# Performance work log

Hardware: AMD Instinct MI355X
Metric: run time of the kernel (lower is better)

Reference implementation:

```python
import jax, jax.numpy as jnp
import numpy as np

H = 8          # num_heads
D_MODEL = 512  # hidden_dim
HEAD_DIM = D_MODEL // H
SCALE = HEAD_DIM ** -0.5
N = 4096
NUM_GRAPHS = 32
NEG_INF = jnp.float32(-jnp.inf)


def setup_inputs() -> dict:
    key = jax.random.key(0)
    ks = jax.random.split(key, 12)
    w_std = D_MODEL ** -0.5  # ~ torch Linear init scale
    inp = {
        "x": jax.random.normal(ks[0], (N, D_MODEL), jnp.float32),
        "attention_bias": jax.random.normal(ks[1], (H, N, N), jnp.float32),
        "batch": jnp.sort(jax.random.randint(ks[2], (N,), 0, NUM_GRAPHS)),
        "Wq": jax.random.normal(ks[3], (D_MODEL, D_MODEL), jnp.float32) * w_std,
        "bq": jax.random.normal(ks[4], (D_MODEL,), jnp.float32) * w_std,
        "Wk": jax.random.normal(ks[5], (D_MODEL, D_MODEL), jnp.float32) * w_std,
        "bk": jax.random.normal(ks[6], (D_MODEL,), jnp.float32) * w_std,
        "Wv": jax.random.normal(ks[7], (D_MODEL, D_MODEL), jnp.float32) * w_std,
        "bv": jax.random.normal(ks[8], (D_MODEL,), jnp.float32) * w_std,
        "Wo": jax.random.normal(ks[9], (D_MODEL, D_MODEL), jnp.float32) * w_std,
        "bo": jax.random.normal(ks[10], (D_MODEL,), jnp.float32) * w_std,
    }
    return inp


def reference(x, attention_bias, batch, Wq, bq, Wk, bk, Wv, bv, Wo, bo):
    n = x.shape[0]
    # projections (torch Linear: y = x @ W.T + b)
    q = (x @ Wq.T + bq).reshape(n, H, HEAD_DIM)
    k = (x @ Wk.T + bk).reshape(n, H, HEAD_DIM)
    v = (x @ Wv.T + bv).reshape(n, H, HEAD_DIM)
    # scores [H, N, N] with relative-PE bias
    attn = jnp.einsum("nhd,mhd->hnm", q, k) * SCALE + attention_bias
    # batch mask: attend only within the same graph
    batch_mask = batch[:, None] != batch[None, :]  # [N, N], True = masked
    attn = jnp.where(batch_mask[None, :, :], NEG_INF, attn)
    attn = jax.nn.softmax(attn, axis=-1)
    attn = jnp.nan_to_num(attn, nan=0.0)
    # dropout is identity in eval / dropout=0.0
    out = jnp.einsum("hnm,mhd->nhd", attn, v).reshape(n, D_MODEL)
    out = out @ Wo.T + bo
    return out
```

## Files before the change

### kernel.cpp

```cpp
#include <hip/hip_runtime.h>

#define NTOK 4096
#define DMODEL 512
#define NHEAD 8
#define HDIM 64
#define KDIM 512
#define KITER (KDIM / 64)

typedef __bf16 bf16x8 __attribute__((ext_vector_type(8)));
typedef float f32x4 __attribute__((ext_vector_type(4)));
typedef unsigned short u16x8 __attribute__((ext_vector_type(8)));
typedef unsigned short u16x4 __attribute__((ext_vector_type(4)));

#define NEGINF (-__builtin_inff())

__device__ __forceinline__ f32x4 mfma16(bf16x8 a, bf16x8 b, f32x4 c) {
  return __builtin_amdgcn_mfma_f32_16x16x32_bf16(a, b, c, 0, 0, 0);
}

__device__ __forceinline__ unsigned short f2bf(float f) {
  unsigned u = __builtin_bit_cast(unsigned, f);
  u += 0x7FFFu + ((u >> 16) & 1u);
  return (unsigned short)(u >> 16);
}

__device__ __forceinline__ void gload_lds16(const void* g, void* l) {
  __builtin_amdgcn_global_load_lds(
      (const __attribute__((address_space(1))) void*)g,
      (__attribute__((address_space(3))) void*)l, 16, 0, 0);
}

__global__ void convert_kernel(const float* __restrict__ x,
                               const float* __restrict__ Wq, const float* __restrict__ bq,
                               const float* __restrict__ Wk, const float* __restrict__ bk,
                               const float* __restrict__ Wv, const float* __restrict__ bv,
                               const float* __restrict__ Wo,
                               const int* __restrict__ batch,
                               unsigned short* __restrict__ xb,
                               unsigned short* __restrict__ wqkv,
                               unsigned short* __restrict__ wo,
                               float* __restrict__ bqkv,
                               int* __restrict__ qrange) {
  __shared__ int bsh[NTOK];
  if (blockIdx.x == 0) {
    for (int i = threadIdx.x; i < NTOK; i += 256) bsh[i] = batch[i];
  }
  const int XV = NTOK * DMODEL / 4;
  const int WV = DMODEL * DMODEL / 4;
  const int total = XV + 4 * WV + 1536 / 4;
  for (int i = blockIdx.x * blockDim.x + threadIdx.x; i < total;
       i += gridDim.x * blockDim.x) {
    if (i < XV) {
      float4 v = ((const float4*)x)[i];
      u16x4 pk = {f2bf(v.x), f2bf(v.y), f2bf(v.z), f2bf(v.w)};
      *(u16x4*)(xb + (size_t)i * 4) = pk;
    } else if (i < XV + 3 * WV) {
      int j = i - XV;
      const float* W; float sc; int jj;
      if (j < WV)          { W = Wq; sc = 0.125f; jj = j; }
      else if (j < 2 * WV) { W = Wk; sc = 1.0f;  jj = j - WV; }
      else                 { W = Wv; sc = 1.0f;  jj = j - 2 * WV; }
      float4 v = ((const float4*)W)[jj];
      u16x4 pk = {f2bf(v.x * sc), f2bf(v.y * sc), f2bf(v.z * sc), f2bf(v.w * sc)};
      *(u16x4*)(wqkv + (size_t)j * 4) = pk;
    } else if (i < XV + 4 * WV) {
      int j = i - XV - 3 * WV;
      float4 v = ((const float4*)Wo)[j];
      u16x4 pk = {f2bf(v.x), f2bf(v.y), f2bf(v.z), f2bf(v.w)};
      *(u16x4*)(wo + (size_t)j * 4) = pk;
    } else {
      int j = (i - XV - 4 * WV) * 4;
      #pragma unroll
      for (int t = 0; t < 4; ++t) {
        int e = j + t;
        float v = (e < 512) ? bq[e] * 0.125f
                 : (e < 1024 ? bk[e - 512] : bv[e - 1024]);
        bqkv[e] = v;
      }
    }
  }
  if (blockIdx.x == 0) {
    __syncthreads();
    if (threadIdx.x < 256) {
      int q0 = threadIdx.x * 16;
      int blo = bsh[q0];
      int bhi = bsh[q0 + 15];
      int lo = 0, hi = NTOK;
      while (lo < hi) { int m = (lo + hi) >> 1; if (bsh[m] < blo) lo = m + 1; else hi = m; }
      qrange[threadIdx.x * 2] = lo >> 6;
      lo = 0; hi = NTOK;
      while (lo < hi) { int m = (lo + hi) >> 1; if (bsh[m] < bhi + 1) lo = m + 1; else hi = m; }
      qrange[threadIdx.x * 2 + 1] = (lo + 63) >> 6;
    }
  }
}

#define BUFE (192 * 64)
#define BUFB (BUFE * 2)
template <int MODE>
__global__ __launch_bounds__(256) void gemm_kernel(
    const unsigned short* __restrict__ A,
    const unsigned short* __restrict__ B,
    const float* __restrict__ biasv,
    float* __restrict__ outf,
    unsigned short* __restrict__ qb,
    unsigned short* __restrict__ kb,
    unsigned short* __restrict__ vt) {
  __shared__ __align__(16) unsigned short lds[3 * BUFE];
  const int tid = threadIdx.x;
  const int lane = tid & 63;
  const int wv = tid >> 6;
  const int wm = wv >> 1, wn = wv & 1;
  const int r16 = lane & 15, g4 = lane >> 4;
  const int mt = blockIdx.x, nt = blockIdx.y;

  f32x4 acc[4][2];
  #pragma unroll
  for (int i = 0; i < 4; ++i)
    #pragma unroll
    for (int j = 0; j < 2; ++j)
      acc[i][j] = (f32x4){0.f, 0.f, 0.f, 0.f};

  const int srow = tid >> 3;
  const int scolb = (tid & 7) << 4;

#define STAGE(KT, BI)                                                        \
  {                                                                          \
    char* bA = (char*)lds + (BI) * BUFB;                                     \
    char* bB = bA + 128 * 128;                                               \
    _Pragma("unroll") for (int i = 0; i < 4; ++i) {                          \
      int row = i * 32 + srow;                                               \
      int cu_ = scolb ^ ((row & 7) << 4);                                    \
      gload_lds16(A + (size_t)(mt * 128 + row) * KDIM + (KT) * 64 + (cu_ >> 1), \
                  bA + i * 4096 + wv * 1024);                                \
    }                                                                        \
    _Pragma("unroll") for (int i = 0; i < 2; ++i) {                          \
      int row = i * 32 + srow;                                               \
      int cu_ = scolb ^ ((row & 7) << 4);                                    \
      gload_lds16(B + (size_t)(nt * 64 + row) * KDIM + (KT) * 64 + (cu_ >> 1), \
                  bB + i * 4096 + wv * 1024);                                \
    }                                                                        \
  }

#define COMPUTE(BI)                                                          \
  {                                                                          \
    const char* base = (const char*)lds + (BI) * BUFB;                       \
    _Pragma("unroll") for (int ks = 0; ks < 2; ++ks) {                       \
      bf16x8 af[4], bfr[2];                                                  \
      _Pragma("unroll") for (int f = 0; f < 4; ++f) {                        \
        int ra = wm * 64 + f * 16 + r16;                                     \
        af[f] = *(const bf16x8*)(base + ra * 128 +                           \
                                 ((ks * 64 + g4 * 16) ^ ((ra & 7) << 4)));   \
      }                                                                      \
      _Pragma("unroll") for (int f = 0; f < 2; ++f) {                        \
        int rb = wn * 32 + f * 16 + r16;                                     \
        bfr[f] = *(const bf16x8*)(base + 128 * 128 + rb * 128 +              \
                                  ((ks * 64 + g4 * 16) ^ ((rb & 7) << 4)));  \
      }                                                                      \
      _Pragma("unroll") for (int fm = 0; fm < 4; ++fm)                       \
        _Pragma("unroll") for (int fn = 0; fn < 2; ++fn)                     \
          acc[fm][fn] = mfma16(af[fm], bfr[fn], acc[fm][fn]);                \
    }                                                                        \
  }

  STAGE(0, 0);
  STAGE(1, 1);
  int cur = 0;
  #pragma unroll
  for (int kt = 0; kt < KITER; ++kt) {
    if (kt < KITER - 1) {
      asm volatile("s_waitcnt vmcnt(6)" ::: "memory");
    } else {
      asm volatile("s_waitcnt vmcnt(0)" ::: "memory");
    }
    __builtin_amdgcn_s_barrier();
    if (kt + 2 < KITER) {
      int bi = cur ? cur - 1 : 2;
      STAGE(kt + 2, bi);
    }
    COMPUTE(cur);
    cur = (cur == 2) ? 0 : cur + 1;
  }
#undef STAGE
#undef COMPUTE

  #pragma unroll
  for (int fm = 0; fm < 4; ++fm) {
    #pragma unroll
    for (int fn = 0; fn < 2; ++fn) {
      int mb = mt * 128 + wm * 64 + fm * 16 + g4 * 4;
      int n = nt * 64 + wn * 32 + fn * 16 + r16;
      float bv = biasv[n];
      if (MODE == 1) {
        #pragma unroll
        for (int r = 0; r < 4; ++r)
          outf[(size_t)(mb + r) * DMODEL + n] = acc[fm][fn][r] + bv;
      } else {
        if (n < 512) {
          #pragma unroll
          for (int r = 0; r < 4; ++r)
            qb[(size_t)(mb + r) * DMODEL + n] = f2bf(acc[fm][fn][r] + bv);
        } else if (n < 1024) {
          int nn = n - 512;
          #pragma unroll
          for (int r = 0; r < 4; ++r)
            kb[(size_t)(mb + r) * DMODEL + nn] = f2bf(acc[fm][fn][r] + bv);
        } else {
          int nn = n - 1024;
          u16x4 pk;
          #pragma unroll
          for (int r = 0; r < 4; ++r) pk[r] = f2bf(acc[fm][fn][r] + bv);
          *(u16x4*)(vt + (size_t)nn * NTOK + mb) = pk;
        }
      }
    }
  }
}

__global__ __launch_bounds__(64) void attn_kernel(
    const unsigned short* __restrict__ qb,
    const unsigned short* __restrict__ kb,
    const unsigned short* __restrict__ vt,
    const float* __restrict__ bias,
    const int* __restrict__ batch,
    const int* __restrict__ qrange,
    unsigned short* __restrict__ ao) {
  __shared__ __align__(16) unsigned short pl[16 * 72];
  const int lane = threadIdx.x & 63;
  const int r16 = lane & 15, g4 = lane >> 4;
  const int h = blockIdx.x & 7;
  const int qt = blockIdx.x >> 3;
  const int qrow0 = qt * 16;
  const int hoff = h * HDIM;

  const unsigned short* qrow = qb + (size_t)(qrow0 + r16) * DMODEL + hoff + g4 * 8;
  bf16x8 qa0 = *(const bf16x8*)qrow;
  bf16x8 qa1 = *(const bf16x8*)(qrow + 32);

  int qbt[4];
  const float* bprow[4];
  const float* bh = bias + (size_t)h * NTOK * NTOK;
  #pragma unroll
  for (int r = 0; r < 4; ++r) {
    qbt[r] = batch[qrow0 + g4 * 4 + r];
    bprow[r] = bh + (size_t)(qrow0 + g4 * 4 + r) * NTOK;
  }

  const int tile0 = qrange[qt * 2];
  const int tile1 = qrange[qt * 2 + 1];

  float m_r[4] = {NEGINF, NEGINF, NEGINF, NEGINF};
  float l_r[4] = {0.f, 0.f, 0.f, 0.f};
  f32x4 o[4];
  #pragma unroll
  for (int d = 0; d < 4; ++d) o[d] = (f32x4){0.f, 0.f, 0.f, 0.f};

#define PREFETCH_KB(T, K0, K1, BV, KBT)                                      \
  {                                                                          \
    int kvb_ = (T) << 6;                                                     \
    _Pragma("unroll") for (int c = 0; c < 4; ++c) {                          \
      const unsigned short* kp =                                             \
          kb + (size_t)(kvb_ + c * 16 + r16) * DMODEL + hoff + g4 * 8;       \
      K0[c] = *(const bf16x8*)kp;                                            \
      K1[c] = *(const bf16x8*)(kp + 32);                                     \
    }                                                                        \
    _Pragma("unroll") for (int c = 0; c < 4; ++c) {                          \
      KBT[c] = batch[kvb_ + c * 16 + r16];                                   \
      _Pragma("unroll") for (int r = 0; r < 4; ++r)                          \
        BV[c][r] = bprow[r][kvb_ + c * 16 + r16];                            \
    }                                                                        \
  }

#define TILE_STEP(T, K0C, K1C, BVC, KBTC, K0N, K1N, BVN, KBTN)               \
  {                                                                          \
    int kvb = (T) << 6;                                                      \
    f32x4 s[4];                                                              \
    _Pragma("unroll") for (int c = 0; c < 4; ++c) {                          \
      f32x4 z = (f32x4){0.f, 0.f, 0.f, 0.f};                                 \
      z = mfma16(qa0, K0C[c], z);                                            \
      z = mfma16(qa1, K1C[c], z);                                            \
      s[c] = z;                                                              \
    }                                                                        \
        \
    bf16x8 v0[4], v1[4];                                                     \
    _Pragma("unroll") for (int d = 0; d < 4; ++d) {                          \
      const unsigned short* vp =                                             \
          vt + (size_t)(hoff + d * 16 + r16) * NTOK + kvb + g4 * 8;          \
      v0[d] = *(const bf16x8*)vp;                                            \
      v1[d] = *(const bf16x8*)(vp + 32);                                     \
    }                                                                        \
     \
    {                                                                        \
      int tn_ = ((T) + 1 < tile1) ? (T) + 1 : (T);                           \
      PREFETCH_KB(tn_, K0N, K1N, BVN, KBTN);                                 \
    }                                                                        \
    _Pragma("unroll") for (int c = 0; c < 4; ++c)                            \
      _Pragma("unroll") for (int r = 0; r < 4; ++r)                          \
        s[c][r] = (qbt[r] == KBTC[c]) ? (s[c][r] + BVC[c][r]) : NEGINF;      \
    float scl[4];                                                            \
    _Pragma("unroll") for (int r = 0; r < 4; ++r) {                          \
      float tm = fmaxf(fmaxf(s[0][r], s[1][r]), fmaxf(s[2][r], s[3][r]));    \
      tm = fmaxf(tm, __shfl_xor(tm, 1));                                     \
      tm = fmaxf(tm, __shfl_xor(tm, 2));                                     \
      tm = fmaxf(tm, __shfl_xor(tm, 4));                                     \
      tm = fmaxf(tm, __shfl_xor(tm, 8));                                     \
      float mn = fmaxf(m_r[r], tm);                                          \
      bool dead = (mn == NEGINF);                                            \
      scl[r] = dead ? 1.0f : __expf(m_r[r] - mn);                            \
      m_r[r] = mn;                                                           \
      float rs = 0.f;                                                        \
      _Pragma("unroll") for (int c = 0; c < 4; ++c) {                        \
        float p = dead ? 0.0f : __expf(s[c][r] - mn);                        \
        s[c][r] = p;                                                         \
        rs += p;                                                             \
      }                                                                      \
      rs += __shfl_xor(rs, 1);                                               \
      rs += __shfl_xor(rs, 2);                                               \
      rs += __shfl_xor(rs, 4);                                               \
      rs += __shfl_xor(rs, 8);                                               \
      l_r[r] = l_r[r] * scl[r] + rs;                                         \
    }                                                                        \
    _Pragma("unroll") for (int c = 0; c < 4; ++c)                            \
      _Pragma("unroll") for (int r = 0; r < 4; ++r)                          \
        pl[(g4 * 4 + r) * 72 + c * 16 + r16] = f2bf(s[c][r]);                \
    asm volatile("" ::: "memory");                                           \
    u16x8 pr0 = *(const u16x8*)(pl + r16 * 72 + g4 * 8);                     \
    u16x8 pr1 = *(const u16x8*)(pl + r16 * 72 + 32 + g4 * 8);                \
    bf16x8 pa0 = __builtin_bit_cast(bf16x8, pr0);                            \
    bf16x8 pa1 = __builtin_bit_cast(bf16x8, pr1);                            \
    _Pragma("unroll") for (int d = 0; d < 4; ++d) {                          \
      _Pragma("unroll") for (int r = 0; r < 4; ++r) o[d][r] *= scl[r];       \
    }                                                                        \
    _Pragma("unroll") for (int d = 0; d < 4; ++d) {                          \
      o[d] = mfma16(pa0, v0[d], o[d]);                                       \
      o[d] = mfma16(pa1, v1[d], o[d]);                                       \
    }                                                                        \
  }

  bf16x8 ka0[4], ka1[4], kc0[4], kc1[4];
  float bva[4][4], bvb[4][4];
  int kta[4], ktb[4];
  PREFETCH_KB(tile0, ka0, ka1, bva, kta);
  int t = tile0;
  while (true) {
    TILE_STEP(t, ka0, ka1, bva, kta, kc0, kc1, bvb, ktb);
    if (++t >= tile1) break;
    TILE_STEP(t, kc0, kc1, bvb, ktb, ka0, ka1, bva, kta);
    if (++t >= tile1) break;
  }

  #pragma unroll
  for (int r = 0; r < 4; ++r) {
    float inv = (l_r[r] > 0.f) ? 1.0f / l_r[r] : 0.0f;
    #pragma unroll
    for (int d = 0; d < 4; ++d)
      ao[(size_t)(qrow0 + g4 * 4 + r) * DMODEL + hoff + d * 16 + r16] =
          f2bf(o[d][r] * inv);
  }
#undef PREFETCH_KB
#undef TILE_STEP
}

extern "C" void kernel_launch(void* const* d_in, const int* in_sizes, int n_in,
                              void* d_out, int out_size, void* d_ws, size_t ws_size,
                              hipStream_t stream) {
  const float* x  = (const float*)d_in[0];
  const float* ab = (const float*)d_in[1];
  const int* batch = (const int*)d_in[2];
  const float* Wq = (const float*)d_in[3];
  const float* bq = (const float*)d_in[4];
  const float* Wk = (const float*)d_in[5];
  const float* bk = (const float*)d_in[6];
  const float* Wv = (const float*)d_in[7];
  const float* bv = (const float*)d_in[8];
  const float* Wo = (const float*)d_in[9];
  const float* bo = (const float*)d_in[10];
  float* out = (float*)d_out;

  char* ws = (char*)d_ws;
  const size_t MB = 1024 * 1024;
  unsigned short* xb   = (unsigned short*)(ws);
  unsigned short* qb   = (unsigned short*)(ws + 4 * MB);
  unsigned short* kb   = (unsigned short*)(ws + 8 * MB);
  unsigned short* vt   = (unsigned short*)(ws + 12 * MB);
  unsigned short* aout = (unsigned short*)(ws + 16 * MB);
  unsigned short* wqkv = (unsigned short*)(ws + 20 * MB);
  unsigned short* wo   = (unsigned short*)(ws + 22 * MB);
  float* bqkv          = (float*)(ws + 23 * MB);
  int* qrange          = (int*)(ws + 23 * MB + 65536);

  convert_kernel<<<dim3(1024), dim3(256), 0, stream>>>(
      x, Wq, bq, Wk, bk, Wv, bv, Wo, batch, xb, wqkv, wo, bqkv, qrange);

  gemm_kernel<0><<<dim3(32, 24), dim3(256), 0, stream>>>(
      xb, wqkv, bqkv, nullptr, qb, kb, vt);

  attn_kernel<<<dim3(2048), dim3(64), 0, stream>>>(
      qb, kb, vt, ab, batch, qrange, aout);

  gemm_kernel<1><<<dim3(32, 8), dim3(256), 0, stream>>>(
      aout, wo, bo, out, nullptr, nullptr, nullptr);
}
```

Before: 54.11 us.

## Use double-buffered GEMM pipeline, smaller out-proj tiles, and MFMA priority hints

The GEMM drops from a three-buffer to a two-buffer LDS pipeline. The output projection uses 64-row tiles and twice as many blocks to fill more CUs. Launch bounds now request more resident blocks per CU. The attention kernel raises wave priority around its MFMA sections with s_setprio. Less prefetch depth may expose load latency in exchange for lower LDS use and higher occupancy.

```diff
diff --git a/kernel.cpp b/kernel.cpp
--- a/kernel.cpp
+++ b/kernel.cpp
@@ -95,10 +95,8 @@
   }
 }
 
-#define BUFE (192 * 64)
-#define BUFB (BUFE * 2)
 template <int MODE>
-__global__ __launch_bounds__(256) void gemm_kernel(
+__global__ __launch_bounds__(256, MODE ? 2 : 3) void gemm_kernel(
     const unsigned short* __restrict__ A,
     const unsigned short* __restrict__ B,
     const float* __restrict__ biasv,
@@ -106,7 +104,11 @@
     unsigned short* __restrict__ qb,
     unsigned short* __restrict__ kb,
     unsigned short* __restrict__ vt) {
-  __shared__ __align__(16) unsigned short lds[3 * BUFE];
+  constexpr int BM = MODE ? 64 : 128;
+  constexpr int FM = MODE ? 2 : 4;
+  constexpr int ALOADS = BM / 32;
+  constexpr int BUFBYTES = (BM + 64) * 64 * 2;
+  __shared__ __align__(16) unsigned short lds[(BM + 64) * 64 * 2];
   const int tid = threadIdx.x;
   const int lane = tid & 63;
   const int wv = tid >> 6;
@@ -114,9 +116,9 @@
   const int r16 = lane & 15, g4 = lane >> 4;
   const int mt = blockIdx.x, nt = blockIdx.y;
 
-  f32x4 acc[4][2];
-  #pragma unroll
-  for (int i = 0; i < 4; ++i)
+  f32x4 acc[FM][2];
+  #pragma unroll
+  for (int i = 0; i < FM; ++i)
     #pragma unroll
     for (int j = 0; j < 2; ++j)
       acc[i][j] = (f32x4){0.f, 0.f, 0.f, 0.f};
@@ -126,12 +128,12 @@
 
 #define STAGE(KT, BI)                                                        \
   {                                                                          \
-    char* bA = (char*)lds + (BI) * BUFB;                                     \
-    char* bB = bA + 128 * 128;                                               \
-    _Pragma("unroll") for (int i = 0; i < 4; ++i) {                          \
+    char* bA = (char*)lds + (BI) * BUFBYTES;                                 \
+    char* bB = bA + BM * 128;                                                \
+    _Pragma("unroll") for (int i = 0; i < ALOADS; ++i) {                     \
       int row = i * 32 + srow;                                               \
       int cu_ = scolb ^ ((row & 7) << 4);                                    \
-      gload_lds16(A + (size_t)(mt * 128 + row) * KDIM + (KT) * 64 + (cu_ >> 1), \
+      gload_lds16(A + (size_t)(mt * BM + row) * KDIM + (KT) * 64 + (cu_ >> 1), \
                   bA + i * 4096 + wv * 1024);                                \
     }                                                                        \
     _Pragma("unroll") for (int i = 0; i < 2; ++i) {                          \
@@ -144,51 +146,49 @@
 
 #define COMPUTE(BI)                                                          \
   {                                                                          \
-    const char* base = (const char*)lds + (BI) * BUFB;                       \
+    const char* base = (const char*)lds + (BI) * BUFBYTES;                   \
     _Pragma("unroll") for (int ks = 0; ks < 2; ++ks) {                       \
-      bf16x8 af[4], bfr[2];                                                  \
-      _Pragma("unroll") for (int f = 0; f < 4; ++f) {                        \
-        int ra = wm * 64 + f * 16 + r16;                                     \
+      bf16x8 af[FM], bfr[2];                                                 \
+      _Pragma("unroll") for (int f = 0; f < FM; ++f) {                       \
+        int ra = wm * (FM * 16) + f * 16 + r16;                              \
         af[f] = *(const bf16x8*)(base + ra * 128 +                           \
                                  ((ks * 64 + g4 * 16) ^ ((ra & 7) << 4)));   \
       }                                                                      \
       _Pragma("unroll") for (int f = 0; f < 2; ++f) {                        \
         int rb = wn * 32 + f * 16 + r16;                                     \
-        bfr[f] = *(const bf16x8*)(base + 128 * 128 + rb * 128 +              \
+        bfr[f] = *(const bf16x8*)(base + BM * 128 + rb * 128 +               \
                                   ((ks * 64 + g4 * 16) ^ ((rb & 7) << 4)));  \
       }                                                                      \
-      _Pragma("unroll") for (int fm = 0; fm < 4; ++fm)                       \
+      _Pragma("unroll") for (int fm = 0; fm < FM; ++fm)                      \
         _Pragma("unroll") for (int fn = 0; fn < 2; ++fn)                     \
           acc[fm][fn] = mfma16(af[fm], bfr[fn], acc[fm][fn]);                \
     }                                                                        \
   }
 
   STAGE(0, 0);
-  STAGE(1, 1);
-  int cur = 0;
   #pragma unroll
   for (int kt = 0; kt < KITER; ++kt) {
-    if (kt < KITER - 1) {
-      asm volatile("s_waitcnt vmcnt(6)" ::: "memory");
+    if (kt + 1 < KITER) {
+      __builtin_amdgcn_s_barrier();
+      STAGE(kt + 1, (kt + 1) & 1);
+      if constexpr (MODE == 0)
+        asm volatile("s_waitcnt vmcnt(6)" ::: "memory");
+      else
+        asm volatile("s_waitcnt vmcnt(4)" ::: "memory");
     } else {
       asm volatile("s_waitcnt vmcnt(0)" ::: "memory");
     }
     __builtin_amdgcn_s_barrier();
-    if (kt + 2 < KITER) {
-      int bi = cur ? cur - 1 : 2;
-      STAGE(kt + 2, bi);
-    }
-    COMPUTE(cur);
-    cur = (cur == 2) ? 0 : cur + 1;
+    COMPUTE(kt & 1);
   }
 #undef STAGE
 #undef COMPUTE
 
   #pragma unroll
-  for (int fm = 0; fm < 4; ++fm) {
+  for (int fm = 0; fm < FM; ++fm) {
     #pragma unroll
     for (int fn = 0; fn < 2; ++fn) {
-      int mb = mt * 128 + wm * 64 + fm * 16 + g4 * 4;
+      int mb = mt * BM + wm * (FM * 16) + fm * 16 + g4 * 4;
       int n = nt * 64 + wn * 32 + fn * 16 + r16;
       float bv = biasv[n];
       if (MODE == 1) {
@@ -275,12 +275,14 @@
   {                                                                          \
     int kvb = (T) << 6;                                                      \
     f32x4 s[4];                                                              \
+    __builtin_amdgcn_s_setprio(1);                                           \
     _Pragma("unroll") for (int c = 0; c < 4; ++c) {                          \
       f32x4 z = (f32x4){0.f, 0.f, 0.f, 0.f};                                 \
       z = mfma16(qa0, K0C[c], z);                                            \
       z = mfma16(qa1, K1C[c], z);                                            \
       s[c] = z;                                                              \
     }                                                                        \
+    __builtin_amdgcn_s_setprio(0);                                           \
         \
     bf16x8 v0[4], v1[4];                                                     \
     _Pragma("unroll") for (int d = 0; d < 4; ++d) {                          \
@@ -331,10 +333,12 @@
     _Pragma("unroll") for (int d = 0; d < 4; ++d) {                          \
       _Pragma("unroll") for (int r = 0; r < 4; ++r) o[d][r] *= scl[r];       \
     }                                                                        \
+    __builtin_amdgcn_s_setprio(1);                                           \
     _Pragma("unroll") for (int d = 0; d < 4; ++d) {                          \
       o[d] = mfma16(pa0, v0[d], o[d]);                                       \
       o[d] = mfma16(pa1, v1[d], o[d]);                                       \
     }                                                                        \
+    __builtin_amdgcn_s_setprio(0);                                           \
   }
 
   bf16x8 ka0[4], ka1[4], kc0[4], kc1[4];
@@ -398,6 +402,6 @@
   attn_kernel<<<dim3(2048), dim3(64), 0, stream>>>(
       qb, kb, vt, ab, batch, qrange, aout);
 
-  gemm_kernel<1><<<dim3(32, 8), dim3(256), 0, stream>>>(
+  gemm_kernel<1><<<dim3(64, 8), dim3(256), 0, stream>>>(
       aout, wo, bo, out, nullptr, nullptr, nullptr);
 }
```

Measured after the change: 51.65 us. 4.6% less time.

## Fuse fp32-to-bf16 conversion into GEMM loads and drop convert kernel

Applied to the files above, without the earlier changes.

Removes the separate convert kernel by having the QKV and output-projection GEMMs load fp32 inputs and weights directly into registers, convert them to bf16 and write them to LDS in a register-staged double buffer. The qrange binary search moves into one block of the QKV GEMM. The output GEMM switches to 64x64 tiles for more blocks, and the attention kernel raises wave priority around its MFMA sections. This saves a launch and an intermediate bf16 round trip, but each GEMM block now re-reads and re-converts fp32 data, doubling global load bytes and adding VALU conversion work in the main loop.

```diff
diff --git a/kernel.cpp b/kernel.cpp
--- a/kernel.cpp
+++ b/kernel.cpp
@@ -24,89 +24,28 @@
   return (unsigned short)(u >> 16);
 }
 
-__device__ __forceinline__ void gload_lds16(const void* g, void* l) {
-  __builtin_amdgcn_global_load_lds(
-      (const __attribute__((address_space(1))) void*)g,
-      (__attribute__((address_space(3))) void*)l, 16, 0, 0);
-}
-
-__global__ void convert_kernel(const float* __restrict__ x,
-                               const float* __restrict__ Wq, const float* __restrict__ bq,
-                               const float* __restrict__ Wk, const float* __restrict__ bk,
-                               const float* __restrict__ Wv, const float* __restrict__ bv,
-                               const float* __restrict__ Wo,
-                               const int* __restrict__ batch,
-                               unsigned short* __restrict__ xb,
-                               unsigned short* __restrict__ wqkv,
-                               unsigned short* __restrict__ wo,
-                               float* __restrict__ bqkv,
-                               int* __restrict__ qrange) {
-  __shared__ int bsh[NTOK];
-  if (blockIdx.x == 0) {
-    for (int i = threadIdx.x; i < NTOK; i += 256) bsh[i] = batch[i];
-  }
-  const int XV = NTOK * DMODEL / 4;
-  const int WV = DMODEL * DMODEL / 4;
-  const int total = XV + 4 * WV + 1536 / 4;
-  for (int i = blockIdx.x * blockDim.x + threadIdx.x; i < total;
-       i += gridDim.x * blockDim.x) {
-    if (i < XV) {
-      float4 v = ((const float4*)x)[i];
-      u16x4 pk = {f2bf(v.x), f2bf(v.y), f2bf(v.z), f2bf(v.w)};
-      *(u16x4*)(xb + (size_t)i * 4) = pk;
-    } else if (i < XV + 3 * WV) {
-      int j = i - XV;
-      const float* W; float sc; int jj;
-      if (j < WV)          { W = Wq; sc = 0.125f; jj = j; }
-      else if (j < 2 * WV) { W = Wk; sc = 1.0f;  jj = j - WV; }
-      else                 { W = Wv; sc = 1.0f;  jj = j - 2 * WV; }
-      float4 v = ((const float4*)W)[jj];
-      u16x4 pk = {f2bf(v.x * sc), f2bf(v.y * sc), f2bf(v.z * sc), f2bf(v.w * sc)};
-      *(u16x4*)(wqkv + (size_t)j * 4) = pk;
-    } else if (i < XV + 4 * WV) {
-      int j = i - XV - 3 * WV;
-      float4 v = ((const float4*)Wo)[j];
-      u16x4 pk = {f2bf(v.x), f2bf(v.y), f2bf(v.z), f2bf(v.w)};
-      *(u16x4*)(wo + (size_t)j * 4) = pk;
-    } else {
-      int j = (i - XV - 4 * WV) * 4;
-      #pragma unroll
-      for (int t = 0; t < 4; ++t) {
-        int e = j + t;
-        float v = (e < 512) ? bq[e] * 0.125f
-                 : (e < 1024 ? bk[e - 512] : bv[e - 1024]);
-        bqkv[e] = v;
-      }
-    }
-  }
-  if (blockIdx.x == 0) {
-    __syncthreads();
-    if (threadIdx.x < 256) {
-      int q0 = threadIdx.x * 16;
-      int blo = bsh[q0];
-      int bhi = bsh[q0 + 15];
-      int lo = 0, hi = NTOK;
-      while (lo < hi) { int m = (lo + hi) >> 1; if (bsh[m] < blo) lo = m + 1; else hi = m; }
-      qrange[threadIdx.x * 2] = lo >> 6;
-      lo = 0; hi = NTOK;
-      while (lo < hi) { int m = (lo + hi) >> 1; if (bsh[m] < bhi + 1) lo = m + 1; else hi = m; }
-      qrange[threadIdx.x * 2 + 1] = (lo + 63) >> 6;
-    }
-  }
-}
-
-#define BUFE (192 * 64)
-#define BUFB (BUFE * 2)
-template <int MODE>
-__global__ __launch_bounds__(256) void gemm_kernel(
-    const unsigned short* __restrict__ A,
-    const unsigned short* __restrict__ B,
-    const float* __restrict__ biasv,
-    float* __restrict__ outf,
+__device__ __forceinline__ int lbound(const int* __restrict__ b, int val) {
+  int lo = 0, hi = NTOK;
+  while (lo < hi) {
+    int mid = (lo + hi) >> 1;
+    if (b[mid] < val) lo = mid + 1; else hi = mid;
+  }
+  return lo;
+}
+
+#define BUFB0 (192 * 64 * 2)
+
+__global__ __launch_bounds__(256, 2) void gemm_qkv(
+    const float* __restrict__ x,
+    const float* __restrict__ Wq, const float* __restrict__ bq,
+    const float* __restrict__ Wk, const float* __restrict__ bk,
+    const float* __restrict__ Wv, const float* __restrict__ bvv,
+    const int* __restrict__ batch,
     unsigned short* __restrict__ qb,
     unsigned short* __restrict__ kb,
-    unsigned short* __restrict__ vt) {
-  __shared__ __align__(16) unsigned short lds[3 * BUFE];
+    unsigned short* __restrict__ vt,
+    int* __restrict__ qrange) {
+  __shared__ __align__(16) unsigned short lds[2 * 192 * 64];
   const int tid = threadIdx.x;
   const int lane = tid & 63;
   const int wv = tid >> 6;
@@ -114,6 +53,10 @@
   const int r16 = lane & 15, g4 = lane >> 4;
   const int mt = blockIdx.x, nt = blockIdx.y;
 
+  const float* WB = (nt < 8) ? Wq : (nt < 16 ? Wk : Wv);
+  const float wscale = (nt < 8) ? 0.125f : 1.0f;
+  const int wrow0 = (nt & 7) * 64;
+
   f32x4 acc[4][2];
   #pragma unroll
   for (int i = 0; i < 4; ++i)
@@ -122,29 +65,51 @@
       acc[i][j] = (f32x4){0.f, 0.f, 0.f, 0.f};
 
   const int srow = tid >> 3;
-  const int scolb = (tid & 7) << 4;
-
-#define STAGE(KT, BI)                                                        \
-  {                                                                          \
-    char* bA = (char*)lds + (BI) * BUFB;                                     \
+  const int c0 = (tid & 7) * 8;
+
+#define LOADR0(KT, RA, RB)                                                   \
+  {                                                                          \
+    _Pragma("unroll") for (int i = 0; i < 4; ++i) {                          \
+      int row = i * 32 + srow;                                               \
+      int cs = c0 ^ ((row & 7) * 8);                                         \
+      const float* src = x + (size_t)(mt * 128 + row) * KDIM + (KT) * 64 + cs;\
+      RA[2 * i]     = *(const f32x4*)src;                                    \
+      RA[2 * i + 1] = *(const f32x4*)(src + 4);                              \
+    }                                                                        \
+    _Pragma("unroll") for (int i = 0; i < 2; ++i) {                          \
+      int row = i * 32 + srow;                                               \
+      int cs = c0 ^ ((row & 7) * 8);                                         \
+      const float* src = WB + (size_t)(wrow0 + row) * KDIM + (KT) * 64 + cs; \
+      RB[2 * i]     = *(const f32x4*)src;                                    \
+      RB[2 * i + 1] = *(const f32x4*)(src + 4);                              \
+    }                                                                        \
+  }
+
+#define WRITER0(BI, RA, RB)                                                  \
+  {                                                                          \
+    char* bA = (char*)lds + (BI) * BUFB0;                                    \
     char* bB = bA + 128 * 128;                                               \
     _Pragma("unroll") for (int i = 0; i < 4; ++i) {                          \
-      int row = i * 32 + srow;                                               \
-      int cu_ = scolb ^ ((row & 7) << 4);                                    \
-      gload_lds16(A + (size_t)(mt * 128 + row) * KDIM + (KT) * 64 + (cu_ >> 1), \
-                  bA + i * 4096 + wv * 1024);                                \
+      u16x8 pk;                                                              \
+      _Pragma("unroll") for (int e = 0; e < 4; ++e) {                        \
+        pk[e]     = f2bf(RA[2 * i][e]);                                      \
+        pk[e + 4] = f2bf(RA[2 * i + 1][e]);                                  \
+      }                                                                      \
+      *(u16x8*)(bA + i * 4096 + tid * 16) = pk;                              \
     }                                                                        \
     _Pragma("unroll") for (int i = 0; i < 2; ++i) {                          \
-      int row = i * 32 + srow;                                               \
-      int cu_ = scolb ^ ((row & 7) << 4);                                    \
-      gload_lds16(B + (size_t)(nt * 64 + row) * KDIM + (KT) * 64 + (cu_ >> 1), \
-                  bB + i * 4096 + wv * 1024);                                \
-    }                                                                        \
-  }
-
-#define COMPUTE(BI)                                                          \
-  {                                                                          \
-    const char* base = (const char*)lds + (BI) * BUFB;                       \
+      u16x8 pk;                                                              \
+      _Pragma("unroll") for (int e = 0; e < 4; ++e) {                        \
+        pk[e]     = f2bf(RB[2 * i][e] * wscale);                             \
+        pk[e + 4] = f2bf(RB[2 * i + 1][e] * wscale);                         \
+      }                                                                      \
+      *(u16x8*)(bB + i * 4096 + tid * 16) = pk;                              \
+    }                                                                        \
+  }
+
+#define COMPUTE0(BI)                                                         \
+  {                                                                          \
+    const char* base = (const char*)lds + (BI) * BUFB0;                      \
     _Pragma("unroll") for (int ks = 0; ks < 2; ++ks) {                       \
       bf16x8 af[4], bfr[2];                                                  \
       _Pragma("unroll") for (int f = 0; f < 4; ++f) {                        \
@@ -163,26 +128,30 @@
     }                                                                        \
   }
 
-  STAGE(0, 0);
-  STAGE(1, 1);
-  int cur = 0;
-  #pragma unroll
-  for (int kt = 0; kt < KITER; ++kt) {
-    if (kt < KITER - 1) {
-      asm volatile("s_waitcnt vmcnt(6)" ::: "memory");
-    } else {
-      asm volatile("s_waitcnt vmcnt(0)" ::: "memory");
-    }
-    __builtin_amdgcn_s_barrier();
-    if (kt + 2 < KITER) {
-      int bi = cur ? cur - 1 : 2;
-      STAGE(kt + 2, bi);
-    }
-    COMPUTE(cur);
-    cur = (cur == 2) ? 0 : cur + 1;
-  }
-#undef STAGE
-#undef COMPUTE
+#define STEP0(KT, RA, RB, RAN, RBN, LAST)                                    \
+  __builtin_amdgcn_s_barrier();                 \
+  WRITER0((KT) & 1, RA, RB);                 \
+  if (!(LAST)) { LOADR0((KT) + 1, RAN, RBN); }                               \
+  __builtin_amdgcn_sched_barrier(0);                                         \
+  asm volatile("s_waitcnt lgkmcnt(0)" ::: "memory");                         \
+  __builtin_amdgcn_s_barrier();              \
+  __builtin_amdgcn_sched_barrier(0);                                         \
+  COMPUTE0((KT) & 1);
+
+  f32x4 rA0[8], rB0[4], rA1[8], rB1[4];
+  LOADR0(0, rA0, rB0);
+  STEP0(0, rA0, rB0, rA1, rB1, 0)
+  STEP0(1, rA1, rB1, rA0, rB0, 0)
+  STEP0(2, rA0, rB0, rA1, rB1, 0)
+  STEP0(3, rA1, rB1, rA0, rB0, 0)
+  STEP0(4, rA0, rB0, rA1, rB1, 0)
+  STEP0(5, rA1, rB1, rA0, rB0, 0)
+  STEP0(6, rA0, rB0, rA1, rB1, 0)
+  STEP0(7, rA1, rB1, rA0, rB0, 1)
+#undef LOADR0
+#undef WRITER0
+#undef COMPUTE0
+#undef STEP0
 
   #pragma unroll
   for (int fm = 0; fm < 4; ++fm) {
@@ -190,29 +159,153 @@
     for (int fn = 0; fn < 2; ++fn) {
       int mb = mt * 128 + wm * 64 + fm * 16 + g4 * 4;
       int n = nt * 64 + wn * 32 + fn * 16 + r16;
-      float bv = biasv[n];
-      if (MODE == 1) {
+      if (n < 512) {
+        float bval = bq[n] * 0.125f;
         #pragma unroll
         for (int r = 0; r < 4; ++r)
-          outf[(size_t)(mb + r) * DMODEL + n] = acc[fm][fn][r] + bv;
+          qb[(size_t)(mb + r) * DMODEL + n] = f2bf(acc[fm][fn][r] + bval);
+      } else if (n < 1024) {
+        int nn = n - 512;
+        float bval = bk[nn];
+        #pragma unroll
+        for (int r = 0; r < 4; ++r)
+          kb[(size_t)(mb + r) * DMODEL + nn] = f2bf(acc[fm][fn][r] + bval);
       } else {
-        if (n < 512) {
-          #pragma unroll
-          for (int r = 0; r < 4; ++r)
-            qb[(size_t)(mb + r) * DMODEL + n] = f2bf(acc[fm][fn][r] + bv);
-        } else if (n < 1024) {
-          int nn = n - 512;
-          #pragma unroll
-          for (int r = 0; r < 4; ++r)
-            kb[(size_t)(mb + r) * DMODEL + nn] = f2bf(acc[fm][fn][r] + bv);
-        } else {
-          int nn = n - 1024;
-          u16x4 pk;
-          #pragma unroll
-          for (int r = 0; r < 4; ++r) pk[r] = f2bf(acc[fm][fn][r] + bv);
-          *(u16x4*)(vt + (size_t)nn * NTOK + mb) = pk;
-        }
+        int nn = n - 1024;
+        float bval = bvv[nn];
+        u16x4 pk;
+        #pragma unroll
+        for (int r = 0; r < 4; ++r) pk[r] = f2bf(acc[fm][fn][r] + bval);
+        *(u16x4*)(vt + (size_t)nn * NTOK + mb) = pk;
       }
+    }
+  }
+
+  if (mt == 0 && nt == 0) {
+    int q0 = tid * 16;
+    if (tid < 256) {
+      int blo = batch[q0];
+      int bhi = batch[q0 + 15];
+      qrange[tid * 2]     = lbound(batch, blo) >> 6;
+      qrange[tid * 2 + 1] = (lbound(batch, bhi + 1) + 63) >> 6;
+    }
+  }
+}
+
+#define BUFB1 (128 * 64 * 2)
+
+__global__ __launch_bounds__(256, 2) void gemm_out(
+    const unsigned short* __restrict__ aout,
+    const float* __restrict__ Wo, const float* __restrict__ bo,
+    float* __restrict__ out) {
+  __shared__ __align__(16) unsigned short lds[2 * 128 * 64];
+  const int tid = threadIdx.x;
+  const int lane = tid & 63;
+  const int wv = tid >> 6;
+  const int wm = wv >> 1, wn = wv & 1;
+  const int r16 = lane & 15, g4 = lane >> 4;
+  const int mt = blockIdx.x, nt = blockIdx.y;
+
+  f32x4 acc[2][2];
+  #pragma unroll
+  for (int i = 0; i < 2; ++i)
+    #pragma unroll
+    for (int j = 0; j < 2; ++j)
+      acc[i][j] = (f32x4){0.f, 0.f, 0.f, 0.f};
+
+  const int srow = tid >> 3;
+  const int c0 = (tid & 7) * 8;
+
+#define LOADR1(KT, RA, RB)                                                   \
+  {                                                                          \
+    _Pragma("unroll") for (int i = 0; i < 2; ++i) {                          \
+      int row = i * 32 + srow;                                               \
+      int cs = c0 ^ ((row & 7) * 8);                                         \
+      RA[i] = *(const u16x8*)(aout + (size_t)(mt * 64 + row) * KDIM +        \
+                              (KT) * 64 + cs);                               \
+    }                                                                        \
+    _Pragma("unroll") for (int i = 0; i < 2; ++i) {                          \
+      int row = i * 32 + srow;                                               \
+      int cs = c0 ^ ((row & 7) * 8);                                         \
+      const float* src = Wo + (size_t)(nt * 64 + row) * KDIM + (KT) * 64 + cs;\
+      RB[2 * i]     = *(const f32x4*)src;                                    \
+      RB[2 * i + 1] = *(const f32x4*)(src + 4);                              \
+    }                                                                        \
+  }
+
+#define WRITER1(BI, RA, RB)                                                  \
+  {                                                                          \
+    char* bA = (char*)lds + (BI) * BUFB1;                                    \
+    char* bB = bA + 64 * 128;                                                \
+    _Pragma("unroll") for (int i = 0; i < 2; ++i)                            \
+      *(u16x8*)(bA + i * 4096 + tid * 16) = RA[i];                           \
+    _Pragma("unroll") for (int i = 0; i < 2; ++i) {                          \
+      u16x8 pk;                                                              \
+      _Pragma("unroll") for (int e = 0; e < 4; ++e) {                        \
+        pk[e]     = f2bf(RB[2 * i][e]);                                      \
+        pk[e + 4] = f2bf(RB[2 * i + 1][e]);                                  \
+      }                                                                      \
+      *(u16x8*)(bB + i * 4096 + tid * 16) = pk;                              \
+    }                                                                        \
+  }
+
+#define COMPUTE1(BI)                                                         \
+  {                                                                          \
+    const char* base = (const char*)lds + (BI) * BUFB1;                      \
+    _Pragma("unroll") for (int ks = 0; ks < 2; ++ks) {                       \
+      bf16x8 af[2], bfr[2];                                                  \
+      _Pragma("unroll") for (int f = 0; f < 2; ++f) {                        \
+        int ra = wm * 32 + f * 16 + r16;                                     \
+        af[f] = *(const bf16x8*)(base + ra * 128 +                           \
+                                 ((ks * 64 + g4 * 16) ^ ((ra & 7) << 4)));   \
+      }                                                                      \
+      _Pragma("unroll") for (int f = 0; f < 2; ++f) {                        \
+        int rb = wn * 32 + f * 16 + r16;                                     \
+        bfr[f] = *(const bf16x8*)(base + 64 * 128 + rb * 128 +               \
+                                  ((ks * 64 + g4 * 16) ^ ((rb & 7) << 4)));  \
+      }                                                                      \
+      _Pragma("unroll") for (int fm = 0; fm < 2; ++fm)                       \
+        _Pragma("unroll") for (int fn = 0; fn < 2; ++fn)                     \
+          acc[fm][fn] = mfma16(af[fm], bfr[fn], acc[fm][fn]);                \
+    }                                                                        \
+  }
+
+#define STEP1(KT, RA, RB, RAN, RBN, LAST)                                    \
+  __builtin_amdgcn_s_barrier();                                              \
+  WRITER1((KT) & 1, RA, RB);                                                 \
+  if (!(LAST)) { LOADR1((KT) + 1, RAN, RBN); }                               \
+  __builtin_amdgcn_sched_barrier(0);                                         \
+  asm volatile("s_waitcnt lgkmcnt(0)" ::: "memory");                         \
+  __builtin_amdgcn_s_barrier();                                              \
+  __builtin_amdgcn_sched_barrier(0);                                         \
+  COMPUTE1((KT) & 1);
+
+  u16x8 rA0[2], rA1[2];
+  f32x4 rB0[4], rB1[4];
+  LOADR1(0, rA0, rB0);
+  STEP1(0, rA0, rB0, rA1, rB1, 0)
+  STEP1(1, rA1, rB1, rA0, rB0, 0)
+  STEP1(2, rA0, rB0, rA1, rB1, 0)
+  STEP1(3, rA1, rB1, rA0, rB0, 0)
+  STEP1(4, rA0, rB0, rA1, rB1, 0)
+  STEP1(5, rA1, rB1, rA0, rB0, 0)
+  STEP1(6, rA0, rB0, rA1, rB1, 0)
+  STEP1(7, rA1, rB1, rA0, rB0, 1)
+#undef LOADR1
+#undef WRITER1
+#undef COMPUTE1
+#undef STEP1
+
+  #pragma unroll
+  for (int fm = 0; fm < 2; ++fm) {
+    #pragma unroll
+    for (int fn = 0; fn < 2; ++fn) {
+      int mb = mt * 64 + wm * 32 + fm * 16 + g4 * 4;
+      int n = nt * 64 + wn * 32 + fn * 16 + r16;
+      float bval = bo[n];
+      #pragma unroll
+      for (int r = 0; r < 4; ++r)
+        out[(size_t)(mb + r) * DMODEL + n] = acc[fm][fn][r] + bval;
     }
   }
 }
@@ -275,13 +368,14 @@
   {                                                                          \
     int kvb = (T) << 6;                                                      \
     f32x4 s[4];                                                              \
+    __builtin_amdgcn_s_setprio(1);                                           \
     _Pragma("unroll") for (int c = 0; c < 4; ++c) {                          \
       f32x4 z = (f32x4){0.f, 0.f, 0.f, 0.f};                                 \
       z = mfma16(qa0, K0C[c], z);                                            \
       z = mfma16(qa1, K1C[c], z);                                            \
       s[c] = z;                                                              \
     }                                                                        \
-        \
+    __builtin_amdgcn_s_setprio(0);                                           \
     bf16x8 v0[4], v1[4];                                                     \
     _Pragma("unroll") for (int d = 0; d < 4; ++d) {                          \
       const unsigned short* vp =                                             \
@@ -289,7 +383,6 @@
       v0[d] = *(const bf16x8*)vp;                                            \
       v1[d] = *(const bf16x8*)(vp + 32);                                     \
     }                                                                        \
-     \
     {                                                                        \
       int tn_ = ((T) + 1 < tile1) ? (T) + 1 : (T);                           \
       PREFETCH_KB(tn_, K0N, K1N, BVN, KBTN);                                 \
@@ -331,10 +424,12 @@
     _Pragma("unroll") for (int d = 0; d < 4; ++d) {                          \
       _Pragma("unroll") for (int r = 0; r < 4; ++r) o[d][r] *= scl[r];       \
     }                                                                        \
+    __builtin_amdgcn_s_setprio(1);                                           \
     _Pragma("unroll") for (int d = 0; d < 4; ++d) {                          \
       o[d] = mfma16(pa0, v0[d], o[d]);                                       \
       o[d] = mfma16(pa1, v1[d], o[d]);                                       \
     }                                                                        \
+    __builtin_amdgcn_s_setprio(0);                                           \
   }
 
   bf16x8 ka0[4], ka1[4], kc0[4], kc1[4];
@@ -379,25 +474,17 @@
 
   char* ws = (char*)d_ws;
   const size_t MB = 1024 * 1024;
-  unsigned short* xb   = (unsigned short*)(ws);
-  unsigned short* qb   = (unsigned short*)(ws + 4 * MB);
-  unsigned short* kb   = (unsigned short*)(ws + 8 * MB);
-  unsigned short* vt   = (unsigned short*)(ws + 12 * MB);
-  unsigned short* aout = (unsigned short*)(ws + 16 * MB);
-  unsigned short* wqkv = (unsigned short*)(ws + 20 * MB);
-  unsigned short* wo   = (unsigned short*)(ws + 22 * MB);
-  float* bqkv          = (float*)(ws + 23 * MB);
-  int* qrange          = (int*)(ws + 23 * MB + 65536);
-
-  convert_kernel<<<dim3(1024), dim3(256), 0, stream>>>(
-      x, Wq, bq, Wk, bk, Wv, bv, Wo, batch, xb, wqkv, wo, bqkv, qrange);
-
-  gemm_kernel<0><<<dim3(32, 24), dim3(256), 0, stream>>>(
-      xb, wqkv, bqkv, nullptr, qb, kb, vt);
+  unsigned short* qb   = (unsigned short*)(ws);
+  unsigned short* kb   = (unsigned short*)(ws + 4 * MB);
+  unsigned short* vt   = (unsigned short*)(ws + 8 * MB);
+  unsigned short* aout = (unsigned short*)(ws + 12 * MB);
+  int* qrange          = (int*)(ws + 16 * MB);
+
+  gemm_qkv<<<dim3(32, 24), dim3(256), 0, stream>>>(
+      x, Wq, bq, Wk, bk, Wv, bv, batch, qb, kb, vt, qrange);
 
   attn_kernel<<<dim3(2048), dim3(64), 0, stream>>>(
       qb, kb, vt, ab, batch, qrange, aout);
 
-  gemm_kernel<1><<<dim3(32, 8), dim3(256), 0, stream>>>(
-      aout, wo, bo, out, nullptr, nullptr, nullptr);
-}
+  gemm_out<<<dim3(64, 8), dim3(256), 0, stream>>>(aout, Wo, bo, out);
+}
```

After: 52.30 us. 3.4% less time.
